# Performance work log

Hardware: AMD Instinct MI355X
Metric: run time of the kernel (lower is better)

Reference implementation:

```python
import jax, jax.numpy as jnp
import numpy as np

N, F_IN, HID, HEADS, E, G, CLS = 20000, 128, 32, 8, 320000, 64, 10


def setup_inputs() -> dict:
    key = jax.random.key(0)
    ks = jax.random.split(key, 16)
    HC = HEADS * HID
    inp = {
        'x': jax.random.normal(ks[0], (N, F_IN), jnp.float32),
        'edge_index': jax.random.randint(ks[1], (2, E), 0, N, jnp.int64),
        'batch': jnp.sort(jax.random.randint(ks[2], (N,), 0, G, jnp.int64)),
        'W1': jax.random.normal(ks[3], (F_IN, HC), jnp.float32) * 0.1,
        'att_l1': jax.random.normal(ks[4], (HEADS, HID), jnp.float32) * 0.1,
        'att_r1': jax.random.normal(ks[5], (HEADS, HID), jnp.float32) * 0.1,
        'b1': jnp.zeros((HC,), jnp.float32),
        'W2': jax.random.normal(ks[6], (HC, HC), jnp.float32) * 0.1,
        'att_l2': jax.random.normal(ks[7], (HEADS, HID), jnp.float32) * 0.1,
        'att_r2': jax.random.normal(ks[8], (HEADS, HID), jnp.float32) * 0.1,
        'b2': jnp.zeros((HC,), jnp.float32),
        'lin_W': jax.random.normal(ks[9], (HC, CLS), jnp.float32) * 0.1,
        'lin_b': jnp.zeros((CLS,), jnp.float32),
    }
    return inp


def _add_self_loops(edge_index):
    loops = jnp.arange(N, dtype=edge_index.dtype)
    return (jnp.concatenate([edge_index[0], loops]),
            jnp.concatenate([edge_index[1], loops]))


def _supergat_conv(x, edge_index, W, att_l, att_r, b):
    # SuperGATConv, attention_type='MX', eval mode (no dropout / neg sampling)
    h = (x @ W).reshape(-1, HEADS, HID)          # [N, H, C]
    src, dst = _add_self_loops(edge_index)       # j -> i
    x_j = h[src]                                 # [Etot, H, C]
    x_i = h[dst]
    logits = jnp.einsum('ehc,ehc->eh', x_i, x_j)            # dot-product part
    alpha = jnp.einsum('ehc,hc->eh', x_j, att_l) + jnp.einsum('ehc,hc->eh', x_i, att_r)
    alpha = alpha * jax.nn.sigmoid(logits)
    alpha = jax.nn.leaky_relu(alpha, 0.2)
    # segment softmax over incoming edges of each dst node
    amax = jax.ops.segment_max(alpha, dst, num_segments=N)
    ex = jnp.exp(alpha - amax[dst])
    denom = jax.ops.segment_sum(ex, dst, num_segments=N)
    attn = ex / (denom[dst] + 1e-16)             # [Etot, H]
    out = jax.ops.segment_sum(x_j * attn[..., None], dst, num_segments=N)  # [N,H,C]
    return out.reshape(-1, HEADS * HID) + b


def reference(x, edge_index, batch, W1, att_l1, att_r1, b1, W2, att_l2, att_r2, b2, lin_W, lin_b):
    h = _supergat_conv(x, edge_index, W1, att_l1, att_r1, b1)
    h = jax.nn.elu(h)
    h = _supergat_conv(h, edge_index, W2, att_l2, att_r2, b2)
    # global mean pool over graphs
    sums = jax.ops.segment_sum(h, batch, num_segments=G)
    cnts = jax.ops.segment_sum(jnp.ones((h.shape[0], 1), h.dtype), batch, num_segments=G)
    pooled = sums / jnp.maximum(cnts, 1.0)
    return pooled @ lin_W + lin_b
```

## Files before the change

kernel.cpp:

```cpp
#include <hip/hip_runtime.h>
#include <hip/hip_bf16.h>
#include <math.h>

#define NNODE 20000
#define FIN   128
#define HC    256
#define HEADS 8
#define HID   32
#define NEDGE 320000
#define ETOT  (NEDGE + NNODE)
#define NGRAPH 64
#define NCLS  10
#define MAXDEG 64

typedef __attribute__((ext_vector_type(8))) short short8v;
typedef __attribute__((ext_vector_type(8))) unsigned short ushort8v;
typedef __attribute__((ext_vector_type(4))) float float4v;

__device__ __forceinline__ ushort f2bf(float f) {
    __hip_bfloat16 b = __float2bfloat16(f);
    return *(ushort*)&b;
}
__device__ __forceinline__ float bf2f(ushort u) {
    return __uint_as_float(((unsigned)u) << 16);
}


#define ZB_DEG ((NNODE + 255) / 256)
#define ZB_BND ((NNODE + 255) / 256)
#define ZB_PS  ((NGRAPH * HC + 255) / 256)

__global__ __launch_bounds__(256) void init_kernel(const float* __restrict__ W1,
                                                   const float* __restrict__ W2,
                                                   const int* __restrict__ batch,
                                                   ushort* __restrict__ W1t,
                                                   ushort* __restrict__ W2t,
                                                   int* __restrict__ deg,
                                                   int* __restrict__ gstart,
                                                   float* __restrict__ psum) {
    int b = blockIdx.x;
    if (b < 128) {
        int e = b * 256 + threadIdx.x;
        int k = e >> 8, n = e & 255;
        W1t[(long)n * FIN + k] = f2bf(W1[(long)k * 256 + n]);
    } else if (b < 384) {
        int e = (b - 128) * 256 + threadIdx.x;
        int k = e >> 8, n = e & 255;
        W2t[(long)n * HC + k] = f2bf(W2[(long)k * 256 + n]);
    } else if (b < 384 + ZB_DEG) {
        int i = (b - 384) * 256 + threadIdx.x;
        if (i < NNODE) deg[i] = 0;
    } else if (b < 384 + ZB_DEG + ZB_BND) {
        int i = (b - 384 - ZB_DEG) * 256 + threadIdx.x;
        if (i < NNODE) {
            int bi = batch[i];
            if (i == 0) {
                for (int g = 0; g <= bi; g++) gstart[g] = 0;
            } else {
                int bp = batch[i - 1];
                for (int g = bp + 1; g <= bi; g++) gstart[g] = i;
            }
            if (i == NNODE - 1) {
                for (int g = bi + 1; g <= NGRAPH; g++) gstart[g] = NNODE;
            }
        }
    } else {
        int i = (b - 384 - ZB_DEG - ZB_BND) * 256 + threadIdx.x;
        if (i < NGRAPH * HC) psum[i] = 0.f;
    }
}


__global__ __launch_bounds__(256) void fill_slots(const int* __restrict__ ei,
                                                  int* __restrict__ deg,
                                                  int* __restrict__ esrc) {
    int e = blockIdx.x * blockDim.x + threadIdx.x;
    if (e >= ETOT) return;
    int src, dst;
    if (e < NEDGE) { src = ei[e]; dst = ei[NEDGE + e]; }
    else           { src = e - NEDGE; dst = src; }
    int slot = atomicAdd(&deg[dst], 1);
    if (slot < MAXDEG) esrc[dst * MAXDEG + slot] = src;
}


template<bool A_FP32>
__global__ __launch_bounds__(256) void gemm_mfma(const void* __restrict__ Aptr,
                                                 const ushort* __restrict__ Bt,
                                                 ushort* __restrict__ C,
                                                 const float* __restrict__ attL,
                                                 const float* __restrict__ attR,
                                                 float* __restrict__ aL,
                                                 float* __restrict__ aR,
                                                 int M, int K) {
    __shared__ __align__(16) ushort As[64][72];
    __shared__ __align__(16) ushort Bs[64][72];
    int tid = threadIdx.x;
    int rowBase = blockIdx.x * 64;
    int colBase = blockIdx.y * 64;
    int wave = tid >> 6;
    int l = tid & 63;
    int lm = l & 15;
    int quad = l >> 4;
    int r0 = (wave >> 1) * 32;
    int c0 = (wave & 1) * 32;

    float4v acc00 = {0.f, 0.f, 0.f, 0.f};
    float4v acc01 = acc00, acc10 = acc00, acc11 = acc00;

    float4  af[4];
    short8v ab[2];
    short8v bb[2];

    auto load_tile = [&](int k0) {
        if constexpr (A_FP32) {
            const float* A = (const float*)Aptr;
            #pragma unroll
            for (int q = 0; q < 4; q++) {
                int idx = tid + q * 256;
                int r   = idx >> 4;
                int kc  = (idx & 15) * 4;
                int grow = rowBase + r;
                float4 v = make_float4(0.f, 0.f, 0.f, 0.f);
                if (grow < M) v = *(const float4*)(A + (long)grow * K + k0 + kc);
                af[q] = v;
            }
        } else {
            const ushort* A = (const ushort*)Aptr;
            #pragma unroll
            for (int q = 0; q < 2; q++) {
                int ch = tid + q * 256;
                int r  = ch >> 3;
                int kc = (ch & 7) * 8;
                int grow = rowBase + r;
                short8v av = {};
                if (grow < M) av = *(const short8v*)(A + (long)grow * K + k0 + kc);
                ab[q] = av;
            }
        }
        #pragma unroll
        for (int q = 0; q < 2; q++) {
            int ch = tid + q * 256;
            int r  = ch >> 3;
            int kc = (ch & 7) * 8;
            bb[q] = *(const short8v*)(Bt + (long)(colBase + r) * K + k0 + kc);
        }
    };

    auto store_tile = [&]() {
        if constexpr (A_FP32) {
            #pragma unroll
            for (int q = 0; q < 4; q++) {
                int idx = tid + q * 256;
                int r   = idx >> 4;
                int kc  = (idx & 15) * 4;
                float4 v = af[q];
                ushort4 o = { f2bf(v.x), f2bf(v.y), f2bf(v.z), f2bf(v.w) };
                *(ushort4*)&As[r][kc] = o;
            }
        } else {
            #pragma unroll
            for (int q = 0; q < 2; q++) {
                int ch = tid + q * 256;
                int r  = ch >> 3;
                int kc = (ch & 7) * 8;
                *(short8v*)&As[r][kc] = ab[q];
            }
        }
        #pragma unroll
        for (int q = 0; q < 2; q++) {
            int ch = tid + q * 256;
            int r  = ch >> 3;
            int kc = (ch & 7) * 8;
            *(short8v*)&Bs[r][kc] = bb[q];
        }
    };

    load_tile(0);
    for (int k0 = 0; k0 < K; k0 += 64) {
        store_tile();
        __syncthreads();
        if (k0 + 64 < K) load_tile(k0 + 64);
        #pragma unroll
        for (int ks = 0; ks < 64; ks += 32) {
            int kb = ks + quad * 8;
            short8v a0 = *(const short8v*)&As[r0 + lm][kb];
            short8v a1 = *(const short8v*)&As[r0 + 16 + lm][kb];
            short8v b0 = *(const short8v*)&Bs[c0 + lm][kb];
            short8v b1 = *(const short8v*)&Bs[c0 + 16 + lm][kb];
            acc00 = __builtin_amdgcn_mfma_f32_16x16x32_bf16(a0, b0, acc00, 0, 0, 0);
            acc01 = __builtin_amdgcn_mfma_f32_16x16x32_bf16(a0, b1, acc01, 0, 0, 0);
            acc10 = __builtin_amdgcn_mfma_f32_16x16x32_bf16(a1, b0, acc10, 0, 0, 0);
            acc11 = __builtin_amdgcn_mfma_f32_16x16x32_bf16(a1, b1, acc11, 0, 0, 0);
        }
        __syncthreads();
    }

    int cb = colBase + c0;
    int hd = cb >> 5;
    float al0 = attL[cb + lm], al1 = attL[cb + 16 + lm];
    float ar0 = attR[cb + lm], ar1 = attR[cb + 16 + lm];
    #pragma unroll
    for (int mi = 0; mi < 2; mi++) {
        float4v s0 = mi ? acc10 : acc00;
        float4v s1 = mi ? acc11 : acc01;
        #pragma unroll
        for (int r = 0; r < 4; r++) {
            int row = rowBase + r0 + mi * 16 + quad * 4 + r;
            float pl = s0[r] * al0 + s1[r] * al1;
            float pr = s0[r] * ar0 + s1[r] * ar1;
            #pragma unroll
            for (int s2 = 1; s2 < 16; s2 <<= 1) {
                pl += __shfl_xor(pl, s2);
                pr += __shfl_xor(pr, s2);
            }
            if (row < M) {
                C[(long)row * 256 + cb + lm]      = f2bf(s0[r]);
                C[(long)row * 256 + cb + 16 + lm] = f2bf(s1[r]);
                if (lm == 0) {
                    aL[row * 8 + hd] = pl;
                    aR[row * 8 + hd] = pr;
                }
            }
        }
    }
}


template<int FUSE_POOL>
__global__ __launch_bounds__(256, 8) void fused_attn(const ushort* __restrict__ h,
                                                     const int* __restrict__ degv,
                                                     const int* __restrict__ esrc,
                                                     const float* __restrict__ aL,
                                                     const float* __restrict__ aR,
                                                     const float* __restrict__ bias,
                                                     ushort* __restrict__ out,
                                                     float* __restrict__ psum,
                                                     const int* __restrict__ batch,
                                                     int apply_elu) {
    __shared__ float sh[4][HC];
    __shared__ int sgid[4];
    int wave = threadIdx.x >> 6;
    int node = blockIdx.x * 4 + wave;
    int l = threadIdx.x & 63;
    int slot = l >> 5;
    int lh = l & 31;
    int head = lh >> 2;

    if (FUSE_POOL && l == 0) sgid[wave] = batch[node];

    const ushort8v* h8 = (const ushort8v*)h;
    ushort8v hiu = h8[(long)node * 32 + lh];
    float a_ri = aR[node * 8 + head];
    int beg = node * MAXDEG;
    int deg = min(degv[node], MAXDEG);

    float lsum = 0.f;
    float acc[8] = {0.f, 0.f, 0.f, 0.f, 0.f, 0.f, 0.f, 0.f};

    int p  = slot;
    int j0 = (p     < deg) ? esrc[beg + p]     : 0;
    int j1 = (p + 2 < deg) ? esrc[beg + p + 2] : 0;
    int j2 = (p + 4 < deg) ? esrc[beg + p + 4] : 0;
    ushort8v hb0 = h8[(long)j0 * 32 + lh];
    float    ab0 = aL[j0 * 8 + head];
    ushort8v hb1 = h8[(long)j1 * 32 + lh];
    float    ab1 = aL[j1 * 8 + head];

    for (; p < deg; p += 2) {
        ushort8v hb2 = h8[(long)j2 * 32 + lh];
        float    ab2 = aL[j2 * 8 + head];
        int j3 = (p + 6 < deg) ? esrc[beg + p + 6] : 0;

        float hj[8];
        float prod = 0.f;
        #pragma unroll
        for (int c = 0; c < 8; c++) {
            hj[c] = bf2f(hb0[c]);
            prod = fmaf(bf2f(hiu[c]), hj[c], prod);
        }
        prod += __shfl_xor(prod, 1);
        prod += __shfl_xor(prod, 2);
        float alpha = (ab0 + a_ri) * __builtin_amdgcn_rcpf(1.f + __expf(-prod));
        alpha = (alpha > 0.f) ? alpha : 0.2f * alpha;
        float ex = __expf(alpha);
        lsum += ex;
        #pragma unroll
        for (int c = 0; c < 8; c++) acc[c] += ex * hj[c];

        hb0 = hb1; ab0 = ab1;
        hb1 = hb2; ab1 = ab2;
        j2  = j3;
    }

    lsum += __shfl_xor(lsum, 32);
    #pragma unroll
    for (int c = 0; c < 8; c++) acc[c] += __shfl_xor(acc[c], 32);

    if (slot == 0) {
        float inv = __builtin_amdgcn_rcpf(lsum + 1e-16f);
        float4 b0 = ((const float4*)bias)[lh * 2];
        float4 b1 = ((const float4*)bias)[lh * 2 + 1];
        float bb[8] = {b0.x, b0.y, b0.z, b0.w, b1.x, b1.y, b1.z, b1.w};
        if (FUSE_POOL) {
            #pragma unroll
            for (int c = 0; c < 8; c++)
                sh[wave][lh * 8 + c] = acc[c] * inv + bb[c];
        } else {
            ushort8v o;
            #pragma unroll
            for (int c = 0; c < 8; c++) {
                float r = acc[c] * inv + bb[c];
                if (apply_elu) r = (r > 0.f) ? r : (__expf(r) - 1.f);
                o[c] = f2bf(r);
            }
            *(ushort8v*)(out + (long)node * 256 + lh * 8) = o;
        }
    }

    if (FUSE_POOL) {
        __syncthreads();
        int t = threadIdx.x;
        float v = sh[0][t];
        int g0 = sgid[0];
        #pragma unroll
        for (int w2 = 1; w2 < 4; w2++) {
            int gw = sgid[w2];
            if (gw == g0) v += sh[w2][t];
            else { atomicAdd(&psum[g0 * HC + t], v); g0 = gw; v = sh[w2][t]; }
        }
        atomicAdd(&psum[g0 * HC + t], v);
    }
}


__global__ __launch_bounds__(256) void final2(const float* __restrict__ psum,
                                              const int* __restrict__ gstart,
                                              const float* __restrict__ linW,
                                              const float* __restrict__ linb,
                                              float* __restrict__ out) {
    int g = blockIdx.x;
    int t = threadIdx.x;
    __shared__ float pooled[HC];
    float cnt = fmaxf((float)(gstart[g + 1] - gstart[g]), 1.f);
    pooled[t] = psum[g * HC + t] / cnt;
    __syncthreads();
    if (t < NCLS) {
        float o = linb[t];
        for (int c = 0; c < HC; c++) o += pooled[c] * linW[c * NCLS + t];
        out[g * NCLS + t] = o;
    }
}


extern "C" void kernel_launch(void* const* d_in, const int* in_sizes, int n_in,
                              void* d_out, int out_size, void* d_ws, size_t ws_size,
                              hipStream_t stream) {
    const float* x     = (const float*)d_in[0];
    const int*   ei    = (const int*)d_in[1];
    const int*   batch = (const int*)d_in[2];
    const float* W1    = (const float*)d_in[3];
    const float* attL1 = (const float*)d_in[4];
    const float* attR1 = (const float*)d_in[5];
    const float* b1    = (const float*)d_in[6];
    const float* W2    = (const float*)d_in[7];
    const float* attL2 = (const float*)d_in[8];
    const float* attR2 = (const float*)d_in[9];
    const float* b2    = (const float*)d_in[10];
    const float* linW  = (const float*)d_in[11];
    const float* linb  = (const float*)d_in[12];
    float* out = (float*)d_out;

    char* w = (char*)d_ws;
    size_t o = 0;
    int* deg    = (int*)(w + o); o += (size_t)NNODE * 4;
    o = (o + 15) & ~(size_t)15;
    int* esrc   = (int*)(w + o); o += (size_t)NNODE * MAXDEG * 4;
    o = (o + 15) & ~(size_t)15;
    ushort* W1t = (ushort*)(w + o); o += (size_t)FIN * HC * 2;
    ushort* W2t = (ushort*)(w + o); o += (size_t)HC * HC * 2;
    o = (o + 15) & ~(size_t)15;
    ushort* hbA = (ushort*)(w + o); o += (size_t)NNODE * HC * 2;
    ushort* hbB = (ushort*)(w + o); o += (size_t)NNODE * HC * 2;
    o = (o + 15) & ~(size_t)15;
    float* aL   = (float*)(w + o); o += (size_t)NNODE * HEADS * 4;
    float* aR   = (float*)(w + o); o += (size_t)NNODE * HEADS * 4;
    o = (o + 15) & ~(size_t)15;
    float* psum = (float*)(w + o); o += (size_t)NGRAPH * HC * 4;
    int* gstart = (int*)(w + o); o += 80 * 4;

    init_kernel<<<384 + ZB_DEG + ZB_BND + ZB_PS, 256, 0, stream>>>(
        W1, W2, batch, W1t, W2t, deg, gstart, psum);

    int eb = (ETOT + 255) / 256;
    fill_slots<<<eb, 256, 0, stream>>>(ei, deg, esrc);

    dim3 gg((NNODE + 63) / 64, HC / 64);
    int ab = (NNODE + 3) / 4;
    gemm_mfma<true><<<gg, 256, 0, stream>>>(x, W1t, hbA, attL1, attR1, aL, aR, NNODE, FIN);
    fused_attn<0><<<ab, 256, 0, stream>>>(hbA, deg, esrc, aL, aR, b1, hbB, nullptr, batch, 1);
    gemm_mfma<false><<<gg, 256, 0, stream>>>(hbB, W2t, hbA, attL2, attR2, aL, aR, NNODE, HC);
    fused_attn<1><<<ab, 256, 0, stream>>>(hbA, deg, esrc, aL, aR, b2, nullptr, psum, batch, 0);
    final2<<<NGRAPH, 256, 0, stream>>>(psum, gstart, linW, linb, out);
}
```

Before: 199.4 us.

## Handle self-loops analytically and store edge sources as 16-bit indices

Self-loop edges are no longer inserted into the adjacency slots. Each node's self-loop term is computed directly from its own features, which the attention kernel already holds, and seeds the softmax accumulators. Edge source indices are stored as ushort instead of int, halving the slot table and its read traffic. This relies on N fitting in 16 bits (20000 does). The slot table also changes which node gets the self-loop when degree overflows MAXDEG, and with no max-subtraction in the softmax the self term changes ordering only slightly.

Result: faster. 195.1 us (-2.2%).

```diff
diff --git a/kernel.cpp b/kernel.cpp
--- a/kernel.cpp
+++ b/kernel.cpp
@@ -8,7 +8,6 @@
 #define HEADS 8
 #define HID   32
 #define NEDGE 320000
-#define ETOT  (NEDGE + NNODE)
 #define NGRAPH 64
 #define NCLS  10
 #define MAXDEG 64
@@ -73,14 +72,13 @@
 
 __global__ __launch_bounds__(256) void fill_slots(const int* __restrict__ ei,
                                                   int* __restrict__ deg,
-                                                  int* __restrict__ esrc) {
+                                                  ushort* __restrict__ esrc) {
     int e = blockIdx.x * blockDim.x + threadIdx.x;
-    if (e >= ETOT) return;
-    int src, dst;
-    if (e < NEDGE) { src = ei[e]; dst = ei[NEDGE + e]; }
-    else           { src = e - NEDGE; dst = src; }
+    if (e >= NEDGE) return;
+    int src = ei[e];
+    int dst = ei[NEDGE + e];
     int slot = atomicAdd(&deg[dst], 1);
-    if (slot < MAXDEG) esrc[dst * MAXDEG + slot] = src;
+    if (slot < MAXDEG) esrc[dst * MAXDEG + slot] = (ushort)src;
 }
 
 
@@ -230,7 +228,7 @@
 template<int FUSE_POOL>
 __global__ __launch_bounds__(256, 8) void fused_attn(const ushort* __restrict__ h,
                                                      const int* __restrict__ degv,
-                                                     const int* __restrict__ esrc,
+                                                     const ushort* __restrict__ esrc,
                                                      const float* __restrict__ aL,
                                                      const float* __restrict__ aR,
                                                      const float* __restrict__ bias,
@@ -252,25 +250,40 @@
     const ushort8v* h8 = (const ushort8v*)h;
     ushort8v hiu = h8[(long)node * 32 + lh];
     float a_ri = aR[node * 8 + head];
+    float a_li = aL[node * 8 + head];
     int beg = node * MAXDEG;
     int deg = min(degv[node], MAXDEG);
 
-    float lsum = 0.f;
-    float acc[8] = {0.f, 0.f, 0.f, 0.f, 0.f, 0.f, 0.f, 0.f};
-
     int p  = slot;
-    int j0 = (p     < deg) ? esrc[beg + p]     : 0;
-    int j1 = (p + 2 < deg) ? esrc[beg + p + 2] : 0;
-    int j2 = (p + 4 < deg) ? esrc[beg + p + 4] : 0;
+    int j0 = (p     < deg) ? (int)esrc[beg + p]     : 0;
+    int j1 = (p + 2 < deg) ? (int)esrc[beg + p + 2] : 0;
+    int j2 = (p + 4 < deg) ? (int)esrc[beg + p + 4] : 0;
     ushort8v hb0 = h8[(long)j0 * 32 + lh];
     float    ab0 = aL[j0 * 8 + head];
     ushort8v hb1 = h8[(long)j1 * 32 + lh];
     float    ab1 = aL[j1 * 8 + head];
 
+    float prod_s = 0.f;
+    #pragma unroll
+    for (int c = 0; c < 8; c++) {
+        float v = bf2f(hiu[c]);
+        prod_s = fmaf(v, v, prod_s);
+    }
+    prod_s += __shfl_xor(prod_s, 1);
+    prod_s += __shfl_xor(prod_s, 2);
+    float alpha_s = (a_li + a_ri) * __builtin_amdgcn_rcpf(1.f + __expf(-prod_s));
+    alpha_s = (alpha_s > 0.f) ? alpha_s : 0.2f * alpha_s;
+    float ex_s = (slot == 0) ? __expf(alpha_s) : 0.f;
+
+    float lsum = ex_s;
+    float acc[8];
+    #pragma unroll
+    for (int c = 0; c < 8; c++) acc[c] = ex_s * bf2f(hiu[c]);
+
     for (; p < deg; p += 2) {
         ushort8v hb2 = h8[(long)j2 * 32 + lh];
         float    ab2 = aL[j2 * 8 + head];
-        int j3 = (p + 6 < deg) ? esrc[beg + p + 6] : 0;
+        int j3 = (p + 6 < deg) ? (int)esrc[beg + p + 6] : 0;
 
         float hj[8];
         float prod = 0.f;
@@ -373,9 +386,9 @@
 
     char* w = (char*)d_ws;
     size_t o = 0;
-    int* deg    = (int*)(w + o); o += (size_t)NNODE * 4;
+    int* deg      = (int*)(w + o); o += (size_t)NNODE * 4;
     o = (o + 15) & ~(size_t)15;
-    int* esrc   = (int*)(w + o); o += (size_t)NNODE * MAXDEG * 4;
+    ushort* esrc  = (ushort*)(w + o); o += (size_t)NNODE * MAXDEG * 2;
     o = (o + 15) & ~(size_t)15;
     ushort* W1t = (ushort*)(w + o); o += (size_t)FIN * HC * 2;
     ushort* W2t = (ushort*)(w + o); o += (size_t)HC * HC * 2;
@@ -392,7 +405,7 @@
     init_kernel<<<384 + ZB_DEG + ZB_BND + ZB_PS, 256, 0, stream>>>(
         W1, W2, batch, W1t, W2t, deg, gstart, psum);
 
-    int eb = (ETOT + 255) / 256;
+    int eb = (NEDGE + 255) / 256;
     fill_slots<<<eb, 256, 0, stream>>>(ei, deg, esrc);
 
     dim3 gg((NNODE + 63) / 64, HC / 64);
```
